# Kernel optimization log

Hardware: AMD Instinct MI355X
Metric: run time of the kernel (lower is better)

The kernel has to match this reference:

```python
import jax, jax.numpy as jnp
import numpy as np

N = 50000      # nodes
E = 800000     # edges (avg degree 16)
IN = 512       # in_channels
H = 128        # hidden_channels
DROP = 0.5     # drop_rate


def setup_inputs() -> dict:
    key = jax.random.key(0)
    k1, k2, k3, k4 = jax.random.split(key, 4)
    feats = jax.random.normal(k1, (N, IN), dtype=jnp.float32)
    # GCNConv learned params (glorot-ish weight, zero bias)
    W = jax.random.normal(k2, (IN, H), dtype=jnp.float32) / np.float32(np.sqrt(IN))
    b = jnp.zeros((H,), dtype=jnp.float32)
    src = jax.random.randint(k3, (E,), 0, N)
    dst = jax.random.randint(k4, (E,), 0, N)
    edge_index = jnp.stack([src, dst]).astype(jnp.int64)
    return {"feats": feats, "W": W, "b": b, "edge_index": edge_index}


def reference(feats, W, b, edge_index):
    n = feats.shape[0]
    loop = jnp.arange(n)
    # add self-loops (PyG GCNConv default)
    src = jnp.concatenate([edge_index[0], loop])
    dst = jnp.concatenate([edge_index[1], loop])
    # symmetric degree normalization over A + I
    deg = jnp.zeros((n,), feats.dtype).at[dst].add(jnp.float32(1.0))
    dinv = jnp.where(deg > 0, jax.lax.rsqrt(deg), jnp.float32(0.0))
    norm = dinv[src] * dinv[dst]  # [E+N]
    x = feats @ W                              # [N, H]
    msgs = x[src] * norm[:, None]              # [E+N, H] gather + scale
    out = jnp.zeros_like(x).at[dst].add(msgs)  # scatter-add aggregate
    out = out + b
    h = jax.nn.relu(out)
    # dropout (training mode), deterministic key
    keep = 1.0 - DROP
    mask = jax.random.bernoulli(jax.random.key(42), keep, h.shape)
    return jnp.where(mask, h / jnp.float32(keep), jnp.float32(0.0))
```

## Files before the change

kernel.cpp:

```cpp
#include <hip/hip_runtime.h>

#define NN 50000
#define NE 800000
#define KIN 512
#define HC 128
#define MAXDEG 64
#define NBK 782
#define BCAP 1536
#define EPB 4096
#define NCH 196

typedef float f32x4 __attribute__((ext_vector_type(4)));
typedef float f32x2 __attribute__((ext_vector_type(2)));
typedef short s16x8 __attribute__((ext_vector_type(8)));

__device__ __forceinline__ ushort f2bf(float f) {
  unsigned u = __float_as_uint(f);
  unsigned r = (u + 0x7FFFu + ((u >> 16) & 1u)) >> 16;
  return (ushort)r;
}

__device__ __forceinline__ void gload_lds16(const void* g, void* l) {
  __builtin_amdgcn_global_load_lds((const __attribute__((address_space(1))) void*)g,
                                   (__attribute__((address_space(3))) void*)l, 16, 0, 0);
}

__device__ __forceinline__ unsigned tf_bits(unsigned i) {
  unsigned x0 = 0u, x1 = i;
  const unsigned ks0 = 0u, ks1 = 42u, ks2 = 0x1BD11BDAu ^ 42u;
#define R(r) { x0 += x1; x1 = (x1 << r) | (x1 >> (32 - r)); x1 ^= x0; }
  x0 += ks0; x1 += ks1;
  R(13) R(15) R(26) R(6)
  x0 += ks1; x1 += ks2 + 1u;
  R(17) R(29) R(16) R(24)
  x0 += ks2; x1 += ks0 + 2u;
  R(13) R(15) R(26) R(6)
  x0 += ks0; x1 += ks1 + 3u;
  R(17) R(29) R(16) R(24)
  x0 += ks1; x1 += ks2 + 4u;
  R(13) R(15) R(26) R(6)
  x0 += ks2; x1 += ks0 + 5u;
#undef R
  return x0 ^ x1;
}

__device__ __forceinline__ void role_map(int bid, int nchg, bool* chain,
                                         int* cid, int* gid) {
  int g8 = bid >> 3, sub = bid & 7;
  if (g8 < 2 * nchg) {
    *chain = ((g8 & 1) == 0);
    int h = g8 >> 1;
    *cid = h * 8 + sub;
    *gid = h * 8 + sub;
  } else {
    *chain = false; *cid = 0;
    *gid = nchg * 8 + (g8 - 2 * nchg) * 8 + sub;
  }
}

__global__ void k_prep(const float* __restrict__ W, ushort* __restrict__ Wt,
                       int* __restrict__ slots, int* __restrict__ bcur) {
  int t = blockIdx.x * 256 + threadIdx.x;
  if (t < NBK) bcur[t] = 0;
  if (t == NBK) slots[NN] = 0;
  if (t < KIN * HC) {
    int c = t & (HC - 1), k = t >> 7;
    Wt[c * KIN + k] = f2bf(W[t]);
  }
}

__device__ void gemm_tile(int g, const float* __restrict__ feats,
                          const ushort* __restrict__ Wt, ushort* __restrict__ xb,
                          unsigned char* __restrict__ mask, char* smem) {
  float*  As = (float*)smem;
  ushort* Bs = (ushort*)(smem + 8192);
  const int tid = threadIdx.x;
  const int lane = tid & 63;
  const int w = tid >> 6;
  const int wm = w >> 1, wn = w & 1;
  const int rbase = g * 32;

  {
    int mb = rbase * 16 + tid;
#pragma unroll
    for (int h = 0; h < 2; ++h, mb += 256) {
      if (mb < NN * 16) {
        unsigned by = 0;
#pragma unroll
        for (int k = 0; k < 8; k++)
          by |= (tf_bits(8u * (unsigned)mb + k) >> 31) << k;
        mask[mb] = (unsigned char)by;
      }
    }
  }

  f32x4 acc[4];
#pragma unroll
  for (int nt = 0; nt < 4; nt++) acc[nt] = f32x4{0.f, 0.f, 0.f, 0.f};

  const int a_rt = w * 8 + (lane >> 4);
  int a_gr[2];
#pragma unroll
  for (int i = 0; i < 2; i++) {
    int gr = rbase + a_rt + i * 4;
    a_gr[i] = (gr < NN) ? gr : NN - 1;
  }
  const int b_ct = w * 32 + (lane >> 3);
  const int b_ch = ((lane & 7) ^ (b_ct & 7)) << 3;

  for (int ks = 0; ks < KIN; ks += 64) {
    __syncthreads();
#pragma unroll
    for (int i = 0; i < 2; i++) {
      int a_ch = ((lane & 15) ^ (a_rt & 7) ^ ((i & 1) << 2)) << 2;
      gload_lds16(feats + (size_t)a_gr[i] * KIN + ks + a_ch,
                  (char*)As + (w * 8 + i * 4) * 256);
    }
#pragma unroll
    for (int i = 0; i < 4; i++)
      gload_lds16(Wt + (size_t)(b_ct + i * 8) * KIN + ks + b_ch,
                  (char*)Bs + (w * 32 + i * 8) * 128);
    __syncthreads();
#pragma unroll
    for (int kk = 0; kk < 2; kk++) {
      s16x8 bfr[4];
#pragma unroll
      for (int nt = 0; nt < 4; nt++) {
        int c = wn * 64 + nt * 16 + (lane & 15);
        int ch = (kk * 4 + (lane >> 4)) ^ (c & 7);
        bfr[nt] = *(const s16x8*)((const char*)Bs + c * 128 + ch * 16);
      }
      int r = wm * 16 + (lane & 15);
      int c0 = kk * 8 + (lane >> 4) * 2;
      f32x4 f0 = *(const f32x4*)((const char*)As + r * 256 + ((c0 ^ (r & 7)) * 16));
      f32x4 f1 = *(const f32x4*)((const char*)As + r * 256 + (((c0 + 1) ^ (r & 7)) * 16));
      s16x8 af;
#pragma unroll
      for (int t = 0; t < 4; t++) {
        af[t]     = (short)f2bf(f0[t]);
        af[t + 4] = (short)f2bf(f1[t]);
      }
#pragma unroll
      for (int nt = 0; nt < 4; nt++)
        acc[nt] = __builtin_amdgcn_mfma_f32_16x16x32_bf16(af, bfr[nt], acc[nt], 0, 0, 0);
    }
  }
  {
    int rb = rbase + wm * 16 + (lane >> 4) * 4;
#pragma unroll
    for (int j = 0; j < 4; j++) {
      int r = rb + j;
      bool ok = (r < NN);
#pragma unroll
      for (int nt = 0; nt < 4; nt++) {
        int c = wn * 64 + nt * 16 + (lane & 15);
        xb[(size_t)r * HC + c] = ok ? f2bf(acc[nt][j]) : (ushort)0;
      }
    }
  }
}

__launch_bounds__(256, 6)
__global__ void k_bg(const float* __restrict__ feats, const ushort* __restrict__ Wt,
                     ushort* __restrict__ xb, const int* __restrict__ ei,
                     int* __restrict__ bcur, unsigned* __restrict__ region,
                     unsigned char* __restrict__ mask) {
  __shared__ __align__(16) char smem[24576];
  bool chain; int cid, gid;
  role_map(blockIdx.x, 25, &chain, &cid, &gid);
  if (chain) {
    if (cid >= NCH) return;
    int* lcnt  = (int*)smem;
    int* gb    = (int*)smem + NBK;
    int* lcnt2 = (int*)smem + 2 * NBK;
    const int tid = threadIdx.x;
    for (int i = tid; i < NBK; i += 256) { lcnt[i] = 0; lcnt2[i] = 0; }
    __syncthreads();
    const int e0 = cid * EPB + tid;
    int dc[16];
#pragma unroll
    for (int k = 0; k < 16; k++) {
      int e = e0 + k * 256;
      dc[k] = (e < NE) ? ei[NE + e] : -1;
    }
#pragma unroll
    for (int k = 0; k < 16; k++)
      if (dc[k] >= 0) atomicAdd(&lcnt[dc[k] >> 6], 1);
    __syncthreads();
    for (int i = tid; i < NBK; i += 256)
      if (lcnt[i]) gb[i] = atomicAdd(&bcur[i], lcnt[i]);
    __syncthreads();
    int sc[16];
#pragma unroll
    for (int k = 0; k < 16; k++) {
      int e = e0 + k * 256;
      sc[k] = (e < NE) ? ei[e] : -1;
    }
#pragma unroll
    for (int k = 0; k < 16; k++) {
      if (dc[k] >= 0) {
        int bkt = dc[k] >> 6;
        int r = atomicAdd(&lcnt2[bkt], 1);
        int p = gb[bkt] + r;
        if (p < BCAP)
          region[(size_t)bkt * BCAP + p] = ((unsigned)dc[k] << 16) | (unsigned)sc[k];
      }
    }
    return;
  }
  if (gid < 1563) gemm_tile(gid, feats, Wt, xb, mask, smem);
}

__global__ void k_csr(const unsigned* __restrict__ region, const int* __restrict__ bcur,
                      ushort* __restrict__ csr16, int* __restrict__ slots) {
  __shared__ int lc[64];
  const int bkt = blockIdx.x;
  const int tid = threadIdx.x;
  if (tid < 64) lc[tid] = 0;
  __syncthreads();
  int cnt = bcur[bkt]; if (cnt > BCAP) cnt = BCAP;
  for (int i = tid; i < cnt; i += 256) {
    unsigned u = region[(size_t)bkt * BCAP + i];
    int d = u >> 16, s = u & 0xFFFFu;
    int slot = atomicAdd(&lc[d & 63], 1);
    if (slot < MAXDEG) csr16[(size_t)d * MAXDEG + slot] = (ushort)s;
  }
  __syncthreads();
  if (tid < 64) {
    int n = bkt * 64 + tid;
    if (n < NN) slots[n] = lc[tid];
  }
}

__global__ void k_agg(const ushort* __restrict__ xb, const int* __restrict__ slots,
                      const ushort* __restrict__ csr16,
                      const unsigned char* __restrict__ mask,
                      const float* __restrict__ b, float* __restrict__ out) {
  int n = blockIdx.x * 4 + (threadIdx.x >> 6);
  if (n >= NN) return;
  const int lane = threadIdx.x & 63;
  const int grp = lane >> 4;
  const int q = lane & 15;
  const int degt = slots[n];
  const int deg = (degt < MAXDEG) ? degt : MAXDEG;
  const float dn = rsqrtf((float)(degt + 1));

  float a0, a1, a2, a3, a4, a5, a6, a7;
  {
    uint4 sv = *(const uint4*)(xb + (size_t)n * HC + q * 8);
    float z = (grp == 0) ? dn : 0.0f;
    a0 = __uint_as_float(sv.x << 16)         * z;
    a1 = __uint_as_float(sv.x & 0xFFFF0000u) * z;
    a2 = __uint_as_float(sv.y << 16)         * z;
    a3 = __uint_as_float(sv.y & 0xFFFF0000u) * z;
    a4 = __uint_as_float(sv.z << 16)         * z;
    a5 = __uint_as_float(sv.z & 0xFFFF0000u) * z;
    a6 = __uint_as_float(sv.w << 16)         * z;
    a7 = __uint_as_float(sv.w & 0xFFFF0000u) * z;
  }

  const ushort* cp = csr16 + (size_t)n * MAXDEG;
  const int np = (deg + 3) >> 2;
  unsigned s0 = (grp < deg) ? cp[grp] : (unsigned)NN;
  uint4 g = *(const uint4*)(xb + (size_t)s0 * HC + q * 8);
  int c0 = slots[s0];
  for (int j = 0; j < np; ++j) {
    int idx = 4 * j + 4 + grp;
    unsigned s1 = (idx < deg) ? cp[idx] : (unsigned)NN;
    uint4 gn = *(const uint4*)(xb + (size_t)s1 * HC + q * 8);
    int c1 = slots[s1];
    float di = rsqrtf((float)(c0 + 1));
    a0 += __uint_as_float(g.x << 16)         * di;
    a1 += __uint_as_float(g.x & 0xFFFF0000u) * di;
    a2 += __uint_as_float(g.y << 16)         * di;
    a3 += __uint_as_float(g.y & 0xFFFF0000u) * di;
    a4 += __uint_as_float(g.z << 16)         * di;
    a5 += __uint_as_float(g.z & 0xFFFF0000u) * di;
    a6 += __uint_as_float(g.w << 16)         * di;
    a7 += __uint_as_float(g.w & 0xFFFF0000u) * di;
    g = gn; c0 = c1;
  }
#define RED(A) A += __shfl_xor(A, 16); A += __shfl_xor(A, 32);
  RED(a0) RED(a1) RED(a2) RED(a3) RED(a4) RED(a5) RED(a6) RED(a7)
#undef RED
  float sx = (grp == 0) ? a0 : (grp == 1) ? a2 : (grp == 2) ? a4 : a6;
  float sy = (grp == 0) ? a1 : (grp == 1) ? a3 : (grp == 2) ? a5 : a7;
  int i0 = n * HC + q * 8 + 2 * grp;
  f32x2 bb = *(const f32x2*)(b + q * 8 + 2 * grp);
  float vx = fmaxf(sx * dn + bb.x, 0.f) * 2.f;
  float vy = fmaxf(sy * dn + bb.y, 0.f) * 2.f;
  unsigned m = mask[n * 16 + q];
  f32x2 r;
  r.x = ((m >> (2 * grp))     & 1u) ? 0.f : vx;
  r.y = ((m >> (2 * grp + 1)) & 1u) ? 0.f : vy;
  *(f32x2*)(out + i0) = r;
}

extern "C" void kernel_launch(void* const* d_in, const int* in_sizes, int n_in,
                              void* d_out, int out_size, void* d_ws, size_t ws_size,
                              hipStream_t stream) {
  const float* feats = (const float*)d_in[0];
  const float* W     = (const float*)d_in[1];
  const float* b     = (const float*)d_in[2];
  const int*   ei    = (const int*)d_in[3];
  float* out = (float*)d_out;

  char* ws = (char*)d_ws;
  size_t o = 0;
  ushort*        xb     = (ushort*)(ws + o);        o += ((size_t)50016 * HC * 2 + 255) & ~(size_t)255;
  ushort*        Wt     = (ushort*)(ws + o);        o += ((size_t)HC * KIN * 2 + 255) & ~(size_t)255;
  int*           slots  = (int*)(ws + o);           o += ((size_t)(NN + 1) * 4 + 255) & ~(size_t)255;
  unsigned char* mask   = (unsigned char*)(ws + o); o += ((size_t)NE + 512 + 255) & ~(size_t)255;
  int*           bcur   = (int*)(ws + o);           o += ((size_t)NBK * 4 + 255) & ~(size_t)255;
  ushort*        csr16  = (ushort*)(ws + o);        o += ((size_t)NN * MAXDEG * 2 + 255) & ~(size_t)255;
  unsigned*      region = (unsigned*)(ws + o);

  k_prep<<<256, 256, 0, stream>>>(W, Wt, slots, bcur);
  k_bg  <<<1763, 256, 0, stream>>>(feats, Wt, xb, ei, bcur, region, mask);
  k_csr <<<NBK, 256, 0, stream>>>(region, bcur, csr16, slots);
  k_agg <<<(NN + 3) / 4, 256, 0, stream>>>(xb, slots, csr16, mask, b, out);
}
```

Baseline: 81.57 us.

## Split fused bucket/GEMM kernel into separate edge-bucketing and GEMM kernels

Replaces the single role-mapped kernel, which interleaved edge-bucketing blocks with GEMM tile blocks, with two separate launches: a bucketing kernel over half-size edge chunks and a dedicated GEMM kernel. This gives each kernel its own shared memory sizing and removes role-dispatch branching, and the smaller chunks spread the bucketing over more blocks. In exchange, bucketing and GEMM no longer overlap on the device, and there is one more kernel launch with a serialization point between them.

```diff
diff --git a/kernel.cpp b/kernel.cpp
--- a/kernel.cpp
+++ b/kernel.cpp
@@ -7,8 +7,8 @@
 #define MAXDEG 64
 #define NBK 782
 #define BCAP 1536
-#define EPB 4096
-#define NCH 196
+#define EPC 2048
+#define NCB 391
 
 typedef float f32x4 __attribute__((ext_vector_type(4)));
 typedef float f32x2 __attribute__((ext_vector_type(2)));
@@ -44,20 +44,6 @@
   return x0 ^ x1;
 }
 
-__device__ __forceinline__ void role_map(int bid, int nchg, bool* chain,
-                                         int* cid, int* gid) {
-  int g8 = bid >> 3, sub = bid & 7;
-  if (g8 < 2 * nchg) {
-    *chain = ((g8 & 1) == 0);
-    int h = g8 >> 1;
-    *cid = h * 8 + sub;
-    *gid = h * 8 + sub;
-  } else {
-    *chain = false; *cid = 0;
-    *gid = nchg * 8 + (g8 - 2 * nchg) * 8 + sub;
-  }
-}
-
 __global__ void k_prep(const float* __restrict__ W, ushort* __restrict__ Wt,
                        int* __restrict__ slots, int* __restrict__ bcur) {
   int t = blockIdx.x * 256 + threadIdx.x;
@@ -69,11 +55,52 @@
   }
 }
 
-__device__ void gemm_tile(int g, const float* __restrict__ feats,
-                          const ushort* __restrict__ Wt, ushort* __restrict__ xb,
-                          unsigned char* __restrict__ mask, char* smem) {
-  float*  As = (float*)smem;
-  ushort* Bs = (ushort*)(smem + 8192);
+__global__ void k_chain(const int* __restrict__ ei, int* __restrict__ bcur,
+                        unsigned* __restrict__ region) {
+  __shared__ int lcnt[NBK];
+  __shared__ int gb[NBK];
+  __shared__ int lcnt2[NBK];
+  const int tid = threadIdx.x;
+  for (int i = tid; i < NBK; i += 256) { lcnt[i] = 0; lcnt2[i] = 0; }
+  __syncthreads();
+  const int e0 = blockIdx.x * EPC + tid;
+  int dc[8];
+#pragma unroll
+  for (int k = 0; k < 8; k++) {
+    int e = e0 + k * 256;
+    dc[k] = (e < NE) ? ei[NE + e] : -1;
+  }
+#pragma unroll
+  for (int k = 0; k < 8; k++)
+    if (dc[k] >= 0) atomicAdd(&lcnt[dc[k] >> 6], 1);
+  __syncthreads();
+  for (int i = tid; i < NBK; i += 256)
+    if (lcnt[i]) gb[i] = atomicAdd(&bcur[i], lcnt[i]);
+  __syncthreads();
+  int sc[8];
+#pragma unroll
+  for (int k = 0; k < 8; k++) {
+    int e = e0 + k * 256;
+    sc[k] = (e < NE) ? ei[e] : -1;
+  }
+#pragma unroll
+  for (int k = 0; k < 8; k++) {
+    if (dc[k] >= 0) {
+      int bkt = dc[k] >> 6;
+      int r = atomicAdd(&lcnt2[bkt], 1);
+      int p = gb[bkt] + r;
+      if (p < BCAP)
+        region[(size_t)bkt * BCAP + p] = ((unsigned)dc[k] << 16) | (unsigned)sc[k];
+    }
+  }
+}
+
+__launch_bounds__(256, 6)
+__global__ void k_gemm(const float* __restrict__ feats, const ushort* __restrict__ Wt,
+                       ushort* __restrict__ xb, unsigned char* __restrict__ mask) {
+  __shared__ __align__(16) float  As[32 * 64];
+  __shared__ __align__(16) ushort Bs[128 * 64];
+  const int g = blockIdx.x;
   const int tid = threadIdx.x;
   const int lane = tid & 63;
   const int w = tid >> 6;
@@ -158,57 +185,6 @@
       }
     }
   }
-}
-
-__launch_bounds__(256, 6)
-__global__ void k_bg(const float* __restrict__ feats, const ushort* __restrict__ Wt,
-                     ushort* __restrict__ xb, const int* __restrict__ ei,
-                     int* __restrict__ bcur, unsigned* __restrict__ region,
-                     unsigned char* __restrict__ mask) {
-  __shared__ __align__(16) char smem[24576];
-  bool chain; int cid, gid;
-  role_map(blockIdx.x, 25, &chain, &cid, &gid);
-  if (chain) {
-    if (cid >= NCH) return;
-    int* lcnt  = (int*)smem;
-    int* gb    = (int*)smem + NBK;
-    int* lcnt2 = (int*)smem + 2 * NBK;
-    const int tid = threadIdx.x;
-    for (int i = tid; i < NBK; i += 256) { lcnt[i] = 0; lcnt2[i] = 0; }
-    __syncthreads();
-    const int e0 = cid * EPB + tid;
-    int dc[16];
-#pragma unroll
-    for (int k = 0; k < 16; k++) {
-      int e = e0 + k * 256;
-      dc[k] = (e < NE) ? ei[NE + e] : -1;
-    }
-#pragma unroll
-    for (int k = 0; k < 16; k++)
-      if (dc[k] >= 0) atomicAdd(&lcnt[dc[k] >> 6], 1);
-    __syncthreads();
-    for (int i = tid; i < NBK; i += 256)
-      if (lcnt[i]) gb[i] = atomicAdd(&bcur[i], lcnt[i]);
-    __syncthreads();
-    int sc[16];
-#pragma unroll
-    for (int k = 0; k < 16; k++) {
-      int e = e0 + k * 256;
-      sc[k] = (e < NE) ? ei[e] : -1;
-    }
-#pragma unroll
-    for (int k = 0; k < 16; k++) {
-      if (dc[k] >= 0) {
-        int bkt = dc[k] >> 6;
-        int r = atomicAdd(&lcnt2[bkt], 1);
-        int p = gb[bkt] + r;
-        if (p < BCAP)
-          region[(size_t)bkt * BCAP + p] = ((unsigned)dc[k] << 16) | (unsigned)sc[k];
-      }
-    }
-    return;
-  }
-  if (gid < 1563) gemm_tile(gid, feats, Wt, xb, mask, smem);
 }
 
 __global__ void k_csr(const unsigned* __restrict__ region, const int* __restrict__ bcur,
@@ -315,8 +291,9 @@
   ushort*        csr16  = (ushort*)(ws + o);        o += ((size_t)NN * MAXDEG * 2 + 255) & ~(size_t)255;
   unsigned*      region = (unsigned*)(ws + o);
 
-  k_prep<<<256, 256, 0, stream>>>(W, Wt, slots, bcur);
-  k_bg  <<<1763, 256, 0, stream>>>(feats, Wt, xb, ei, bcur, region, mask);
-  k_csr <<<NBK, 256, 0, stream>>>(region, bcur, csr16, slots);
-  k_agg <<<(NN + 3) / 4, 256, 0, stream>>>(xb, slots, csr16, mask, b, out);
-}
+  k_prep <<<256, 256, 0, stream>>>(W, Wt, slots, bcur);
+  k_chain<<<NCB, 256, 0, stream>>>(ei, bcur, region);
+  k_gemm <<<1563, 256, 0, stream>>>(feats, Wt, xb, mask);
+  k_csr  <<<NBK, 256, 0, stream>>>(region, bcur, csr16, slots);
+  k_agg  <<<(NN + 3) / 4, 256, 0, stream>>>(xb, slots, csr16, mask, b, out);
+}
```

Result: slower. 93.63 us (+14.8%).
